# Kernel optimization log

Measured on AMD Instinct MI355X. Metric: run time of the kernel, lower is better.

Reference implementation:

```python
import jax, jax.numpy as jnp
import numpy as np
from math import comb

N, D, ORDER, P = 32768, 8, 19, 20
O = ORDER + 1


def bernstein(X, order):
    # X: [N, D] in [0,1] -> Bernstein basis [N, D, order+1]
    o = order + 1
    r = jnp.arange(o, dtype=X.dtype)
    binom = jnp.asarray([comb(order, k) for k in range(o)], dtype=X.dtype)
    Xe = X[..., None]
    return (Xe ** r) * ((1.0 - Xe) ** (order - r)) * binom


def setup_inputs() -> dict:
    key = jax.random.key(0)
    k0, k1, k2, k3, k4, k5 = jax.random.split(key, 6)
    X = jax.random.uniform(k0, (N, D), dtype=jnp.float32)
    # perm: each row is a permutation of range(D) (as in the module default)
    perm = jax.vmap(lambda k: jax.random.permutation(k, D))(jax.random.split(k1, P)).astype(jnp.int32)
    meanw0 = -0.2 + 0.1 * jax.random.normal(k2, (P, 1, O), dtype=jnp.float32)
    meanw = -0.2 + 0.1 * jax.random.normal(k3, (D - 1, P, O, O), dtype=jnp.float32)
    varw0 = 0.05 * jax.random.normal(k4, (P, 1, O), dtype=jnp.float32)
    varw = 0.05 * jax.random.normal(k5, (D - 1, P, O, O), dtype=jnp.float32)
    return {"X": X, "perm": perm, "meanw0": meanw0, "meanw": meanw,
            "varw0": varw0, "varw": varw}


def reference(X, perm, meanw0, meanw, varw0, varw):
    outB = bernstein(X, ORDER)                       # [N, D, O]
    outBp = jnp.transpose(outB[:, perm], (1, 0, 2, 3))  # gather axis=1 -> [P, N, D, O]

    # ---- f_mean: chain of small matmuls with exp(meanw_i), gated by basis ----
    f = jnp.exp(meanw0) * outBp[:, :, 0, :]          # [P,1,O]*[P,N,O] -> [P,N,O]
    for i in range(1, D):
        f = jnp.einsum('pno,poq->pnq', f, jnp.exp(meanw[i - 1])) * outBp[:, :, i, :]
    mean = jnp.sum(jnp.sum(f, axis=-1), axis=0)[:, None]   # [N,1]

    # ---- f_var: six moment chains one..six, exp(meanw)^2 * exp(varw)^k ----
    kk = jnp.arange(1, 7, dtype=X.dtype).reshape(6, 1, 1, 1)
    B2_0 = outBp[:, :, 0, :] ** 2                    # [P,N,O]
    acc = jnp.exp(2.0 * meanw0 + kk * varw0) * B2_0[None]  # [6,P,N,O]
    for i in range(1, D):
        Wi = jnp.exp(2.0 * meanw[i - 1] + kk * varw[i - 1])  # [6,P,O,O]
        acc = jnp.einsum('kpno,kpoq->kpnq', acc, Wi) * (outBp[:, :, i, :] ** 2)[None]
    mom = jnp.sum(acc, axis=-1)                      # [6,P,N]
    c = jnp.asarray([1.0, 1 / 2, 1 / 6, 1 / 24, 1 / 120, 1 / 720], dtype=X.dtype)
    var = jnp.einsum('k,kpn->n', c, mom)[:, None]    # [N,1]

    return jnp.concatenate([mean, var], axis=-1)     # [N,2]
```

## Files before the change

### kernel.cpp

```cpp
#include <hip/hip_runtime.h>
#include <math.h>

#define NPTS 32768
#define DD 8
#define OO 20
#define PP 20
#define NCHAIN 7
#define NT 2

typedef _Float16 half8 __attribute__((ext_vector_type(8)));
typedef __fp16 fp16x2 __attribute__((ext_vector_type(2)));
typedef float floatx16 __attribute__((ext_vector_type(16)));
typedef unsigned int u32;

#define AS1 __attribute__((address_space(1)))
#define AS3 __attribute__((address_space(3)))

__device__ __forceinline__ int sigma_row(int m) {
    return (m >= 4 && m < 12) ? (m ^ 12) : m;
}

__device__ __forceinline__ void basis20(float tv, float* g) {
    constexpr float binom[OO] = {
        1.f, 19.f, 171.f, 969.f, 3876.f, 11628.f, 27132.f, 50388.f, 75582.f,
        92378.f, 92378.f, 75582.f, 50388.f, 27132.f, 11628.f, 3876.f, 969.f,
        171.f, 19.f, 1.f};
    float a = tv, b = 1.f - tv, v = 1.f;
#pragma unroll
    for (int q = 0; q < OO; ++q) { g[q] = v; v *= a; }
    v = 1.f;
#pragma unroll
    for (int q = OO - 1; q >= 0; --q) { g[q] = g[q] * v * binom[q]; v *= b; }
}

__device__ __forceinline__ unsigned pk2rtn(float a, float b) {
    union { _Float16 h[2]; unsigned u; } cv;
    cv.h[0] = (_Float16)a; cv.h[1] = (_Float16)b;
    return cv.u;
}

__device__ __forceinline__ unsigned pack_pk(float x, float y) {
    union { fp16x2 h; unsigned u; } cv;
    cv.h = __builtin_amdgcn_cvt_pkrtz(x, y);
    return cv.u;
}

__device__ __forceinline__ fp16x2 u2h(unsigned u) {
    union { unsigned u; fp16x2 h; } c; c.u = u; return c.h;
}
__device__ __forceinline__ unsigned h2u(fp16x2 h) {
    union { unsigned u; fp16x2 h; } c; c.h = h; return c.u;
}

__global__ void prep_kernel(const float* __restrict__ X,
                            const float* __restrict__ meanw0,
                            const float* __restrict__ meanw,
                            const float* __restrict__ varw0,
                            const float* __restrict__ varw,
                            float* __restrict__ W0,
                            _Float16* __restrict__ WA,
                            unsigned* __restrict__ G) {
    int e = blockIdx.x * 256 + threadIdx.x;
    const int n0 = NCHAIN * PP * OO;
    const int nW = NCHAIN * (DD - 1) * PP * 32 * 32;
    const int nG = NPTS * DD;
    if (e < n0) {
        int q = e % OO;
        int rem = e / OO;
        int p = rem % PP;
        int c = rem / PP;
        float m = meanw0[p * OO + q];
        W0[e] = (c == 0) ? __expf(m) : __expf(2.f * m + (float)c * varw0[p * OO + q]);
    } else if (e < n0 + nW) {
        int idx = e - n0;
        int j = idx & 7; idx >>= 3;
        int l = idx & 63; idx >>= 6;
        int f = idx & 1; idx >>= 1;
        int p = idx % PP; idx /= PP;
        int i = idx % (DD - 1);
        int c = idx / (DD - 1);
        int m = l & 31;
        int k = (l >> 5) * 8 + f * 16 + j;
        int q = sigma_row(m);
        float v = 0.f;
        if (q < OO && k < OO) {
            int mi = ((i * PP + p) * OO + k) * OO + q;
            float mm = meanw[mi];
            v = (c == 0) ? __expf(mm) : __expf(2.f * mm + (float)c * varw[mi]);
        }
        WA[e - n0] = (_Float16)v;
    } else if (e < n0 + nW + nG) {
        int idx = e - n0 - nW;
        int n = idx & (NPTS - 1);
        int d = idx >> 15;
        float g[OO];
        basis20(X[(size_t)n * DD + d], g);
        float lo[12], hi12[12];
#pragma unroll
        for (int r = 0; r < 8; ++r) lo[r] = g[r];
#pragma unroll
        for (int r = 0; r < 4; ++r) lo[8 + r] = g[16 + r];
#pragma unroll
        for (int r = 0; r < 8; ++r) hi12[r] = g[8 + r];
#pragma unroll
        for (int r = 0; r < 4; ++r) hi12[8 + r] = 0.f;
        unsigned rec[24];
#pragma unroll
        for (int q = 0; q < 6; ++q) {
            rec[q]      = pk2rtn(lo[2 * q], lo[2 * q + 1]);
            rec[6 + q]  = pk2rtn(lo[2 * q] * lo[2 * q], lo[2 * q + 1] * lo[2 * q + 1]);
            rec[12 + q] = pk2rtn(hi12[2 * q], hi12[2 * q + 1]);
            rec[18 + q] = pk2rtn(hi12[2 * q] * hi12[2 * q], hi12[2 * q + 1] * hi12[2 * q + 1]);
        }
        uint4* out = (uint4*)(G + (size_t)(d * NPTS + n) * 24);
#pragma unroll
        for (int q = 0; q < 6; ++q) out[q] = ((const uint4*)rec)[q];
    }
}

__global__ __launch_bounds__(256, 2) void chain_kernel(
    const int* __restrict__ perm,
    const float* __restrict__ W0, const _Float16* __restrict__ WA,
    const unsigned* __restrict__ G, float* __restrict__ partial) {
    const int lane = threadIdx.x & 63;
    const int wv = threadIdx.x >> 6;
    const int nl = lane & 31;
    const bool hi = (lane >> 5) != 0;
    const int n0 = (blockIdx.x * 4 + wv) * (32 * NT);
    const int p = blockIdx.y;
    const int goff = hi ? 12 : 0;

    __shared__ __align__(16) _Float16 Alds[2][NCHAIN * 1024];

    int dp[DD];
#pragma unroll
    for (int i = 0; i < DD; ++i) dp[i] = perm[p * DD + i];

    const unsigned uz = ((unsigned)dp[0]) >> 20;
    const float fz = __uint_as_float(uz);
    floatx16 kZero;
#pragma unroll
    for (int r = 0; r < 16; ++r) kZero[r] = fz;

    {
        const _Float16* wbase = WA + (size_t)p * 1024;
#pragma unroll
        for (int u = wv; u < 2 * NCHAIN; u += 4) {
            int c = u >> 1, h = u & 1;
            const _Float16* src =
                wbase + (size_t)c * (DD - 1) * PP * 1024 + h * 512 + lane * 8;
            __builtin_amdgcn_global_load_lds(
                (const AS1 u32*)src, (AS3 u32*)&Alds[0][u * 512], 16, 0, 0);
        }
    }

    unsigned st[NT][NCHAIN][6];

#pragma unroll
    for (int tile = 0; tile < NT; ++tile) {
        const uint4* rp = (const uint4*)(
            G + ((size_t)dp[0] * NPTS + (n0 + tile * 32 + nl)) * 24 + goff);
        uint4 r0 = rp[0], r1 = rp[1], r2 = rp[2];
        unsigned gw[6] = {r0.x, r0.y, r0.z, r0.w, r1.x, r1.y};
        unsigned sw[6] = {r1.z, r1.w, r2.x, r2.y, r2.z, r2.w};
        float gcf[12], scf[12];
#pragma unroll
        for (int q = 0; q < 6; ++q) {
            fp16x2 gh = u2h(gw[q]), sh = u2h(sw[q]);
            gcf[2 * q] = (float)gh.x; gcf[2 * q + 1] = (float)gh.y;
            scf[2 * q] = (float)sh.x; scf[2 * q + 1] = (float)sh.y;
        }
#pragma unroll
        for (int c = 0; c < NCHAIN; ++c) {
            const float* w0r = W0 + (c * PP + p) * OO;
            float val[12];
#pragma unroll
            for (int r = 0; r < 8; ++r) {
                float ws = hi ? w0r[r + 8] : w0r[r];
                val[r] = ws * (c == 0 ? gcf[r] : scf[r]);
            }
#pragma unroll
            for (int r = 8; r < 12; ++r) {
                float ws = hi ? 0.f : w0r[r + 8];
                val[r] = ws * (c == 0 ? gcf[r] : scf[r]);
            }
#pragma unroll
            for (int e = 0; e < 6; ++e)
                st[tile][c][e] = pack_pk(val[2 * e], val[2 * e + 1]);
        }
    }

    const float coef[NCHAIN] = {0.f, 1.f, 0.5f, 1.f / 6.f, 1.f / 24.f,
                                1.f / 120.f, 1.f / 720.f};
    float sm[NT], sv[NT];
#pragma unroll
    for (int tile = 0; tile < NT; ++tile) { sm[tile] = 0.f; sv[tile] = 0.f; }

    __syncthreads();

#pragma unroll
    for (int i = 1; i < DD; ++i) {
        const int cur = (i - 1) & 1;

        if (i < DD - 1) {
            const _Float16* wbase = WA + (size_t)(i * PP + p) * 1024;
#pragma unroll
            for (int u = wv; u < 2 * NCHAIN; u += 4) {
                int c = u >> 1, h = u & 1;
                const _Float16* src =
                    wbase + (size_t)c * (DD - 1) * PP * 1024 + h * 512 + lane * 8;
                __builtin_amdgcn_global_load_lds(
                    (const AS1 u32*)src, (AS3 u32*)&Alds[cur ^ 1][u * 512], 16, 0, 0);
            }
        }

        unsigned gw[NT][6], sw[NT][6];
#pragma unroll
        for (int tile = 0; tile < NT; ++tile) {
            const uint4* rp = (const uint4*)(
                G + ((size_t)dp[i] * NPTS + (n0 + tile * 32 + nl)) * 24 + goff);
            uint4 r0 = rp[0], r1 = rp[1], r2 = rp[2];
            gw[tile][0] = r0.x; gw[tile][1] = r0.y; gw[tile][2] = r0.z;
            gw[tile][3] = r0.w; gw[tile][4] = r1.x; gw[tile][5] = r1.y;
            sw[tile][0] = r1.z; sw[tile][1] = r1.w; sw[tile][2] = r2.x;
            sw[tile][3] = r2.y; sw[tile][4] = r2.z; sw[tile][5] = r2.w;
        }

        float gcf[NT][12], scf[NT][12];
        if (i == DD - 1) {
#pragma unroll
            for (int tile = 0; tile < NT; ++tile)
#pragma unroll
                for (int q = 0; q < 6; ++q) {
                    fp16x2 gh = u2h(gw[tile][q]), sh = u2h(sw[tile][q]);
                    gcf[tile][2 * q] = (float)gh.x; gcf[tile][2 * q + 1] = (float)gh.y;
                    scf[tile][2 * q] = (float)sh.x; scf[tile][2 * q + 1] = (float)sh.y;
                }
        }

#pragma unroll
        for (int c = 0; c < NCHAIN; ++c) {
            const _Float16* ab = &Alds[cur][c * 1024 + lane * 8];
            half8 A0 = *(const half8*)(ab);
            half8 A1 = *(const half8*)(ab + 512);

#pragma unroll
            for (int tile = 0; tile < NT; ++tile) {
                union { unsigned u[4]; half8 h; } B0, B1;
                B0.u[0] = st[tile][c][0]; B0.u[1] = st[tile][c][1];
                B0.u[2] = st[tile][c][2]; B0.u[3] = st[tile][c][3];
                B1.u[0] = st[tile][c][4]; B1.u[1] = st[tile][c][5];
                B1.u[2] = uz;             B1.u[3] = uz;

                floatx16 acc;
                acc = __builtin_amdgcn_mfma_f32_32x32x16_f16(A0, B0.h, kZero, 0, 0, 0);
                acc = __builtin_amdgcn_mfma_f32_32x32x16_f16(A1, B1.h, acc, 0, 0, 0);

                if (i < DD - 1) {
#pragma unroll
                    for (int e = 0; e < 6; ++e) {
                        fp16x2 pr = __builtin_amdgcn_cvt_pkrtz(acc[2 * e], acc[2 * e + 1]);
                        fp16x2 gv = u2h(c == 0 ? gw[tile][e] : sw[tile][e]);
                        st[tile][c][e] = h2u(pr * gv);
                    }
                } else {
                    float s = 0.f;
#pragma unroll
                    for (int r = 0; r < 12; ++r)
                        s += acc[r] * (c == 0 ? gcf[tile][r] : scf[tile][r]);
                    if (c == 0) sm[tile] = s;
                    else        sv[tile] += coef[c] * s;
                }
            }
        }

        if (i < DD - 1) __syncthreads();
    }

#pragma unroll
    for (int tile = 0; tile < NT; ++tile) {
        float m = sm[tile] + __shfl_xor(sm[tile], 32, 64);
        float v = sv[tile] + __shfl_xor(sv[tile], 32, 64);
        if (lane < 32) {
            partial[(size_t)p * NPTS + n0 + tile * 32 + nl] = m;
            partial[(size_t)(PP + p) * NPTS + n0 + tile * 32 + nl] = v;
        }
    }
}

__global__ void reduce_kernel(const float* __restrict__ partial,
                              float* __restrict__ out) {
    int n = blockIdx.x * 256 + threadIdx.x;
    float m = 0.f, v = 0.f;
#pragma unroll
    for (int p = 0; p < PP; ++p) {
        m += partial[(size_t)p * NPTS + n];
        v += partial[(size_t)(PP + p) * NPTS + n];
    }
    out[2 * n] = m;
    out[2 * n + 1] = v;
}

extern "C" void kernel_launch(void* const* d_in, const int* in_sizes, int n_in,
                              void* d_out, int out_size, void* d_ws, size_t ws_size,
                              hipStream_t stream) {
    const float* X      = (const float*)d_in[0];
    const int*   perm   = (const int*)d_in[1];
    const float* meanw0 = (const float*)d_in[2];
    const float* meanw  = (const float*)d_in[3];
    const float* varw0  = (const float*)d_in[4];
    const float* varw   = (const float*)d_in[5];
    float* out = (float*)d_out;

    float*     W0      = (float*)d_ws;
    _Float16*  WA      = (_Float16*)((char*)d_ws + 11200);
    float*     partial = (float*)((char*)d_ws + 11200 + 2007040);
    unsigned*  G       = (unsigned*)((char*)d_ws + 11200 + 2007040 + 5242880);

    int prep_n = NCHAIN * PP * OO + NCHAIN * (DD - 1) * PP * 32 * 32 + NPTS * DD;
    hipLaunchKernelGGL(prep_kernel, dim3((prep_n + 255) / 256), dim3(256), 0,
                       stream, X, meanw0, meanw, varw0, varw, W0, WA, G);

    dim3 grid(NPTS / (128 * NT), PP);
    hipLaunchKernelGGL(chain_kernel, grid, dim3(256), 0, stream,
                       perm, W0, WA, G, partial);

    hipLaunchKernelGGL(reduce_kernel, dim3(NPTS / 256), dim3(256), 0, stream,
                       partial, out);
}
```

Baseline: 158.4 us.

## Halve basis record size by squaring on the fly and replace reduce with atomics

The prep kernel now stores only the fp16 basis values, 12 words per point-dimension instead of 24. The chain kernel squares them in registers (packed fp16 multiply for the chain states, fp32 for the final gate), halving the gather traffic through G. The partial buffer and reduce kernel are replaced by a zero-fill kernel plus float atomicAdd of per-permutation results into the output. The trade-offs are 20-way atomic contention per output element, non-deterministic summation order, and squares rounded in fp16 rather than fp32.

```diff
diff --git a/kernel.cpp b/kernel.cpp
--- a/kernel.cpp
+++ b/kernel.cpp
@@ -50,6 +50,11 @@
 }
 __device__ __forceinline__ unsigned h2u(fp16x2 h) {
     union { unsigned u; fp16x2 h; } c; c.h = h; return c.u;
+}
+
+__global__ void zero_kernel(float4* __restrict__ out) {
+    int e = blockIdx.x * 256 + threadIdx.x;
+    out[e] = make_float4(0.f, 0.f, 0.f, 0.f);
 }
 
 __global__ void prep_kernel(const float* __restrict__ X,
@@ -95,40 +100,35 @@
         int d = idx >> 15;
         float g[OO];
         basis20(X[(size_t)n * DD + d], g);
-        float lo[12], hi12[12];
-#pragma unroll
-        for (int r = 0; r < 8; ++r) lo[r] = g[r];
-#pragma unroll
-        for (int r = 0; r < 4; ++r) lo[8 + r] = g[16 + r];
-#pragma unroll
-        for (int r = 0; r < 8; ++r) hi12[r] = g[8 + r];
-#pragma unroll
-        for (int r = 0; r < 4; ++r) hi12[8 + r] = 0.f;
-        unsigned rec[24];
-#pragma unroll
-        for (int q = 0; q < 6; ++q) {
-            rec[q]      = pk2rtn(lo[2 * q], lo[2 * q + 1]);
-            rec[6 + q]  = pk2rtn(lo[2 * q] * lo[2 * q], lo[2 * q + 1] * lo[2 * q + 1]);
-            rec[12 + q] = pk2rtn(hi12[2 * q], hi12[2 * q + 1]);
-            rec[18 + q] = pk2rtn(hi12[2 * q] * hi12[2 * q], hi12[2 * q + 1] * hi12[2 * q + 1]);
-        }
-        uint4* out = (uint4*)(G + (size_t)(d * NPTS + n) * 24);
-#pragma unroll
-        for (int q = 0; q < 6; ++q) out[q] = ((const uint4*)rec)[q];
+        uint4 o0, o1, o2;
+        o0.x = pk2rtn(g[0], g[1]);
+        o0.y = pk2rtn(g[2], g[3]);
+        o0.z = pk2rtn(g[4], g[5]);
+        o0.w = pk2rtn(g[6], g[7]);
+        o1.x = pk2rtn(g[16], g[17]);
+        o1.y = pk2rtn(g[18], g[19]);
+        o1.z = pk2rtn(g[8], g[9]);
+        o1.w = pk2rtn(g[10], g[11]);
+        o2.x = pk2rtn(g[12], g[13]);
+        o2.y = pk2rtn(g[14], g[15]);
+        o2.z = 0u;
+        o2.w = 0u;
+        uint4* out = (uint4*)(G + (size_t)(d * NPTS + n) * 12);
+        out[0] = o0; out[1] = o1; out[2] = o2;
     }
 }
 
 __global__ __launch_bounds__(256, 2) void chain_kernel(
     const int* __restrict__ perm,
     const float* __restrict__ W0, const _Float16* __restrict__ WA,
-    const unsigned* __restrict__ G, float* __restrict__ partial) {
+    const unsigned* __restrict__ G, float* __restrict__ out) {
     const int lane = threadIdx.x & 63;
     const int wv = threadIdx.x >> 6;
     const int nl = lane & 31;
     const bool hi = (lane >> 5) != 0;
     const int n0 = (blockIdx.x * 4 + wv) * (32 * NT);
     const int p = blockIdx.y;
-    const int goff = hi ? 12 : 0;
+    const int goffd = hi ? 6 : 0;
 
     __shared__ __align__(16) _Float16 Alds[2][NCHAIN * 1024];
 
@@ -158,18 +158,18 @@
 
 #pragma unroll
     for (int tile = 0; tile < NT; ++tile) {
-        const uint4* rp = (const uint4*)(
-            G + ((size_t)dp[0] * NPTS + (n0 + tile * 32 + nl)) * 24 + goff);
-        uint4 r0 = rp[0], r1 = rp[1], r2 = rp[2];
-        unsigned gw[6] = {r0.x, r0.y, r0.z, r0.w, r1.x, r1.y};
-        unsigned sw[6] = {r1.z, r1.w, r2.x, r2.y, r2.z, r2.w};
+        const uint2* rp = (const uint2*)(
+            G + ((size_t)dp[0] * NPTS + (n0 + tile * 32 + nl)) * 12 + goffd);
+        uint2 r0 = rp[0], r1 = rp[1], r2 = rp[2];
+        unsigned gw[6] = {r0.x, r0.y, r1.x, r1.y, r2.x, r2.y};
         float gcf[12], scf[12];
 #pragma unroll
         for (int q = 0; q < 6; ++q) {
-            fp16x2 gh = u2h(gw[q]), sh = u2h(sw[q]);
+            fp16x2 gh = u2h(gw[q]);
             gcf[2 * q] = (float)gh.x; gcf[2 * q + 1] = (float)gh.y;
-            scf[2 * q] = (float)sh.x; scf[2 * q + 1] = (float)sh.y;
-        }
+        }
+#pragma unroll
+        for (int r = 0; r < 12; ++r) scf[r] = gcf[r] * gcf[r];
 #pragma unroll
         for (int c = 0; c < NCHAIN; ++c) {
             const float* w0r = W0 + (c * PP + p) * OO;
@@ -217,25 +217,36 @@
         unsigned gw[NT][6], sw[NT][6];
 #pragma unroll
         for (int tile = 0; tile < NT; ++tile) {
-            const uint4* rp = (const uint4*)(
-                G + ((size_t)dp[i] * NPTS + (n0 + tile * 32 + nl)) * 24 + goff);
-            uint4 r0 = rp[0], r1 = rp[1], r2 = rp[2];
-            gw[tile][0] = r0.x; gw[tile][1] = r0.y; gw[tile][2] = r0.z;
-            gw[tile][3] = r0.w; gw[tile][4] = r1.x; gw[tile][5] = r1.y;
-            sw[tile][0] = r1.z; sw[tile][1] = r1.w; sw[tile][2] = r2.x;
-            sw[tile][3] = r2.y; sw[tile][4] = r2.z; sw[tile][5] = r2.w;
+            const uint2* rp = (const uint2*)(
+                G + ((size_t)dp[i] * NPTS + (n0 + tile * 32 + nl)) * 12 + goffd);
+            uint2 r0 = rp[0], r1 = rp[1], r2 = rp[2];
+            gw[tile][0] = r0.x; gw[tile][1] = r0.y;
+            gw[tile][2] = r1.x; gw[tile][3] = r1.y;
+            gw[tile][4] = r2.x; gw[tile][5] = r2.y;
+        }
+        if (i < DD - 1) {
+#pragma unroll
+            for (int tile = 0; tile < NT; ++tile)
+#pragma unroll
+                for (int e = 0; e < 6; ++e) {
+                    fp16x2 gh = u2h(gw[tile][e]);
+                    sw[tile][e] = h2u(gh * gh);
+                }
         }
 
         float gcf[NT][12], scf[NT][12];
         if (i == DD - 1) {
 #pragma unroll
-            for (int tile = 0; tile < NT; ++tile)
+            for (int tile = 0; tile < NT; ++tile) {
 #pragma unroll
                 for (int q = 0; q < 6; ++q) {
-                    fp16x2 gh = u2h(gw[tile][q]), sh = u2h(sw[tile][q]);
+                    fp16x2 gh = u2h(gw[tile][q]);
                     gcf[tile][2 * q] = (float)gh.x; gcf[tile][2 * q + 1] = (float)gh.y;
-                    scf[tile][2 * q] = (float)sh.x; scf[tile][2 * q + 1] = (float)sh.y;
                 }
+#pragma unroll
+                for (int r = 0; r < 12; ++r)
+                    scf[tile][r] = gcf[tile][r] * gcf[tile][r];
+            }
         }
 
 #pragma unroll
@@ -282,23 +293,11 @@
         float m = sm[tile] + __shfl_xor(sm[tile], 32, 64);
         float v = sv[tile] + __shfl_xor(sv[tile], 32, 64);
         if (lane < 32) {
-            partial[(size_t)p * NPTS + n0 + tile * 32 + nl] = m;
-            partial[(size_t)(PP + p) * NPTS + n0 + tile * 32 + nl] = v;
-        }
-    }
-}
-
-__global__ void reduce_kernel(const float* __restrict__ partial,
-                              float* __restrict__ out) {
-    int n = blockIdx.x * 256 + threadIdx.x;
-    float m = 0.f, v = 0.f;
-#pragma unroll
-    for (int p = 0; p < PP; ++p) {
-        m += partial[(size_t)p * NPTS + n];
-        v += partial[(size_t)(PP + p) * NPTS + n];
-    }
-    out[2 * n] = m;
-    out[2 * n + 1] = v;
+            int n = n0 + tile * 32 + nl;
+            atomicAdd(&out[2 * n], m);
+            atomicAdd(&out[2 * n + 1], v);
+        }
+    }
 }
 
 extern "C" void kernel_launch(void* const* d_in, const int* in_sizes, int n_in,
@@ -312,19 +311,18 @@
     const float* varw   = (const float*)d_in[5];
     float* out = (float*)d_out;
 
-    float*     W0      = (float*)d_ws;
-    _Float16*  WA      = (_Float16*)((char*)d_ws + 11200);
-    float*     partial = (float*)((char*)d_ws + 11200 + 2007040);
-    unsigned*  G       = (unsigned*)((char*)d_ws + 11200 + 2007040 + 5242880);
+    float*     W0 = (float*)d_ws;
+    _Float16*  WA = (_Float16*)((char*)d_ws + 11200);
+    unsigned*  G  = (unsigned*)((char*)d_ws + 11200 + 2007040);
 
     int prep_n = NCHAIN * PP * OO + NCHAIN * (DD - 1) * PP * 32 * 32 + NPTS * DD;
     hipLaunchKernelGGL(prep_kernel, dim3((prep_n + 255) / 256), dim3(256), 0,
                        stream, X, meanw0, meanw, varw0, varw, W0, WA, G);
 
+    hipLaunchKernelGGL(zero_kernel, dim3(2 * NPTS / (4 * 256)), dim3(256), 0,
+                       stream, (float4*)out);
+
     dim3 grid(NPTS / (128 * NT), PP);
     hipLaunchKernelGGL(chain_kernel, grid, dim3(256), 0, stream,
-                       perm, W0, WA, G, partial);
-
-    hipLaunchKernelGGL(reduce_kernel, dim3(NPTS / 256), dim3(256), 0, stream,
-                       partial, out);
-}
+                       perm, W0, WA, G, out);
+}
```

Measured after the change: 143.4 us. -9.5%, faster.
